# Kernel tuning notes

Measured on AMD Instinct MI355X. Metric: run time of the kernel, lower is better.

Reference implementation:

```python
import jax, jax.numpy as jnp
import numpy as np

N_CHEM = 200000
N_DIS = 200000
D = 256
L = 2  # num_layers
R = 4  # relations: 0=cause(chem->dis),1=relate(chem->dis),2=rev_relate(dis->chem),3=child(dis->dis)
E = 500000


def setup_inputs() -> dict:
    key = jax.random.key(0)
    ks = jax.random.split(key, 12)
    x_chem = jax.random.normal(ks[0], (N_CHEM, D), dtype=jnp.float32)
    x_dis = jax.random.normal(ks[1], (N_DIS, D), dtype=jnp.float32)
    ei_cause = jax.random.randint(ks[2], (2, E), 0, N_CHEM, dtype=jnp.int32)
    ei_relate = jax.random.randint(ks[3], (2, E), 0, N_CHEM, dtype=jnp.int32)
    ei_rev = jax.random.randint(ks[4], (2, E), 0, N_DIS, dtype=jnp.int32)
    ei_child = jax.random.randint(ks[5], (2, E), 0, N_DIS, dtype=jnp.int32)
    scale = 1.0 / np.sqrt(D)
    # PyG SAGEConv params per (layer, relation): lin_l (W+b, applied to mean-aggregated
    # neighbors) and lin_r (W only, applied to destination/root features).
    Wl = jax.random.normal(ks[6], (L, R, D, D), dtype=jnp.float32) * scale
    bl = jnp.zeros((L, R, D), dtype=jnp.float32)
    Wr = jax.random.normal(ks[7], (L, R, D, D), dtype=jnp.float32) * scale
    return {"x_chem": x_chem, "x_dis": x_dis, "Wl": Wl, "bl": bl, "Wr": Wr,
            "ei_cause": ei_cause, "ei_relate": ei_relate, "ei_rev": ei_rev,
            "ei_child": ei_child}


def _sage(x_src, x_dst, ei, Wl, bl, Wr, n_dst):
    # SAGEConv: lin_l(mean_{j in N(i)} x_j) + lin_r(x_i)
    src, dst = ei[0], ei[1]
    msg = jnp.take(x_src, src, axis=0)                      # [E, D] gather
    s = jax.ops.segment_sum(msg, dst, num_segments=n_dst)   # [n_dst, D]
    cnt = jax.ops.segment_sum(jnp.ones((ei.shape[1],), x_src.dtype), dst,
                              num_segments=n_dst)
    mean = s / jnp.maximum(cnt, 1.0)[:, None]               # zero-degree -> 0
    return mean @ Wl + bl + x_dst @ Wr


def _hetero_layer(x_chem, x_dis, Wl, bl, Wr, ei_cause, ei_relate, ei_rev, ei_child):
    # HeteroConv(aggr='sum'): sum conv outputs per destination node type.
    out_dis = (_sage(x_chem, x_dis, ei_cause, Wl[0], bl[0], Wr[0], N_DIS)
               + _sage(x_chem, x_dis, ei_relate, Wl[1], bl[1], Wr[1], N_DIS)
               + _sage(x_dis, x_dis, ei_child, Wl[3], bl[3], Wr[3], N_DIS))
    out_chem = _sage(x_dis, x_chem, ei_rev, Wl[2], bl[2], Wr[2], N_CHEM)
    return out_chem, out_dis


def reference(x_chem, x_dis, Wl, bl, Wr, ei_cause, ei_relate, ei_rev, ei_child):
    # layers[:-1]: conv -> relu -> dropout(p=0, identity)
    for l in range(L - 1):
        x_chem, x_dis = _hetero_layer(x_chem, x_dis, Wl[l], bl[l], Wr[l],
                                      ei_cause, ei_relate, ei_rev, ei_child)
        x_chem = jax.nn.relu(x_chem)
        x_dis = jax.nn.relu(x_dis)
    # last layer: conv only
    x_chem, x_dis = _hetero_layer(x_chem, x_dis, Wl[L - 1], bl[L - 1], Wr[L - 1],
                                  ei_cause, ei_relate, ei_rev, ei_child)
    return x_chem, x_dis
```

## Files before the change

### kernel.cpp

```cpp
#include <hip/hip_runtime.h>

#define D_FEAT 256
constexpr int N_CHEM = 200000;
constexpr int N_DIS  = 200000;
constexpr int N_EDGE = 500000;
constexpr int NROWS  = 200000;
constexpr int NPAD   = 200064;

typedef _Float16 f16x8 __attribute__((ext_vector_type(8)));
typedef _Float16 f16x4 __attribute__((ext_vector_type(4)));
typedef float    f32x4 __attribute__((ext_vector_type(4)));

__device__ __forceinline__ void gload_lds16(const void* g, void* l) {
    __builtin_amdgcn_global_load_lds(
        (const __attribute__((address_space(1))) void*)g,
        (__attribute__((address_space(3))) void*)l, 16, 0, 0);
}

__global__ __launch_bounds__(256) void counti_k(const int* __restrict__ ei,
                                                int* __restrict__ cnt, int nE) {
    int e = blockIdx.x * 256 + threadIdx.x;
    if (e < nE) atomicAdd(&cnt[ei[nE + e]], 1);
}

__global__ __launch_bounds__(256) void scan1_k(const int* __restrict__ cnt,
                                               int* __restrict__ offs,
                                               int* __restrict__ bsums, int n) {
    __shared__ int s[256];
    const int t = threadIdx.x;
    const int i = blockIdx.x * 256 + t;
    const int v = (i < n) ? cnt[i] : 0;
    s[t] = v;
    __syncthreads();
#pragma unroll
    for (int d = 1; d < 256; d <<= 1) {
        const int x = (t >= d) ? s[t - d] : 0;
        __syncthreads();
        s[t] += x;
        __syncthreads();
    }
    if (i < n) offs[i] = s[t] - v;
    if (t == 255) bsums[blockIdx.x] = s[255];
}

__global__ __launch_bounds__(1024) void scan2_k(int* __restrict__ bsums, int nb) {
    __shared__ int s[1024];
    const int t = threadIdx.x;
    const int v = (t < nb) ? bsums[t] : 0;
    s[t] = v;
    __syncthreads();
#pragma unroll
    for (int d = 1; d < 1024; d <<= 1) {
        const int x = (t >= d) ? s[t - d] : 0;
        __syncthreads();
        s[t] += x;
        __syncthreads();
    }
    if (t < nb) bsums[t] = s[t] - v;
}

__global__ __launch_bounds__(256) void scan3_k(int* __restrict__ offs,
                                               int* __restrict__ cursor,
                                               const int* __restrict__ bsums, int n) {
    const int i = blockIdx.x * 256 + threadIdx.x;
    if (i < n) {
        const int v = offs[i] + bsums[blockIdx.x];
        offs[i] = v;
        cursor[i] = v;
    }
}

__global__ __launch_bounds__(256) void fill_k(const int* __restrict__ ei,
                                              int* __restrict__ cursor,
                                              int* __restrict__ csr, int nE) {
    int e = blockIdx.x * 256 + threadIdx.x;
    if (e < nE) {
        const int d = ei[nE + e];
        const int p = atomicAdd(&cursor[d], 1);
        csr[p] = ei[e];
    }
}

__global__ __launch_bounds__(256) void wt_k(const float* __restrict__ Wl,
                                            const float* __restrict__ Wr,
                                            const float* __restrict__ bl,
                                            _Float16* __restrict__ WT_dis,
                                            _Float16* __restrict__ WT_chem,
                                            float* __restrict__ bsum, int l) {
    const int idx = blockIdx.x * 256 + threadIdx.x;
    const float* Wl_l = Wl + (size_t)l * 4 * 65536;
    const float* Wr_l = Wr + (size_t)l * 4 * 65536;
    if (idx < 262144) {
        const int n = idx >> 10, k = idx & 1023, seg = k >> 8, kk = k & 255;
        float v;
        if (seg == 0)
            v = Wr_l[kk * 256 + n] + Wr_l[65536 + kk * 256 + n] + Wr_l[3 * 65536 + kk * 256 + n];
        else if (seg == 1) v = Wl_l[kk * 256 + n];
        else if (seg == 2) v = Wl_l[65536 + kk * 256 + n];
        else               v = Wl_l[3 * 65536 + kk * 256 + n];
        WT_dis[(size_t)l * 262144 + idx] = (_Float16)v;
    } else if (idx < 393216) {
        const int li = idx - 262144;
        const int n = li >> 9, k = li & 511, seg = k >> 8, kk = k & 255;
        const float v = (seg == 0) ? Wr_l[2 * 65536 + kk * 256 + n]
                                   : Wl_l[2 * 65536 + kk * 256 + n];
        WT_chem[(size_t)l * 131072 + li] = (_Float16)v;
    } else if (idx < 393216 + 256) {
        const int n = idx - 393216;
        const float* b = bl + (size_t)l * 1024;
        bsum[l * 256 + n] = b[n] + b[256 + n] + b[3 * 256 + n];
    }
}

__global__ __launch_bounds__(256) void cvt16_k(const float* __restrict__ in,
                                               _Float16* __restrict__ out, int n4) {
    int i = blockIdx.x * 256 + threadIdx.x;
    if (i < n4) {
        const float4 v = reinterpret_cast<const float4*>(in)[i];
        f16x4 o;
        o[0] = (_Float16)v.x; o[1] = (_Float16)v.y;
        o[2] = (_Float16)v.z; o[3] = (_Float16)v.w;
        reinterpret_cast<f16x4*>(out)[i] = o;
    }
}

__global__ __launch_bounds__(256) void gather_k(const _Float16* __restrict__ x,
                                                const int* __restrict__ csr,
                                                const int* __restrict__ offs,
                                                const int* __restrict__ cnt,
                                                _Float16* __restrict__ agg,
                                                int base, int rows) {
    const int wid = threadIdx.x >> 6;
    const int lane = threadIdx.x & 63;
    const int grp = lane >> 4;
    const int li  = lane & 15;
    const int lrow = blockIdx.x * 16 + wid * 4 + grp;
    if (lrow >= rows) return;
    const int row = base + lrow;
    const int start = offs[row];
    const int n = cnt[row];
    float a0[8] = {0,0,0,0,0,0,0,0}, a1[8] = {0,0,0,0,0,0,0,0};
    const _Float16* xb = x + li * 16;
    for (int j = 0; j < n; ++j) {
        const int s = csr[start + j];
        const f16x8 v0 = *reinterpret_cast<const f16x8*>(xb + (size_t)s * D_FEAT);
        const f16x8 v1 = *reinterpret_cast<const f16x8*>(xb + (size_t)s * D_FEAT + 8);
#pragma unroll
        for (int q = 0; q < 8; ++q) { a0[q] += (float)v0[q]; a1[q] += (float)v1[q]; }
    }
    const float inv = 1.0f / fmaxf((float)n, 1.0f);
    f16x8 o0, o1;
#pragma unroll
    for (int q = 0; q < 8; ++q) {
        o0[q] = (_Float16)(a0[q] * inv);
        o1[q] = (_Float16)(a1[q] * inv);
    }
    _Float16* ap = agg + (size_t)lrow * D_FEAT + li * 16;
    *reinterpret_cast<f16x8*>(ap) = o0;
    *reinterpret_cast<f16x8*>(ap + 8) = o1;
}

template <int NSEG, bool RELU_OUT>
__global__ __launch_bounds__(256) void gemml_k(
    const _Float16* __restrict__ A0, const _Float16* __restrict__ A1,
    const _Float16* __restrict__ A2, const _Float16* __restrict__ A3,
    const _Float16* __restrict__ WT, const float* __restrict__ bias,
    float* __restrict__ Cf, _Float16* __restrict__ Ch, int vrows) {
    constexpr int KT = NSEG * 256;
    constexpr int NS = KT / 64;
    __shared__ _Float16 Asl[2][128 * 64];
    __shared__ _Float16 Bsl[2][128 * 64];
    const int t = threadIdx.x;
    const int w = t >> 6, l = t & 63;
    const int wm = w & 1, wn = w >> 1;
    const int fr = l & 15, ko = (l >> 4) << 3;
    const int row0 = blockIdx.x * 128;
    const int col0 = blockIdx.y * 128;

    f32x4 acc[4][4];
#pragma unroll
    for (int m = 0; m < 4; ++m)
#pragma unroll
        for (int n = 0; n < 4; ++n) acc[m][n] = f32x4{0.f, 0.f, 0.f, 0.f};

    const int srow = t >> 3;
    const int schk = t & 7;
    const int gchk = schk ^ (srow & 7);
    const int rsw  = (fr & 7) << 3;

    auto STAGE = [&](int buf, int ks) {
        const int seg = ks >> 2;
        const _Float16* Ab = (seg == 0) ? A0 : ((seg == 1) ? A1 : ((seg == 2) ? A2 : A3));
        const int kofs = ((ks & 3) << 6) + gchk * 8;
#pragma unroll
        for (int is = 0; is < 4; ++is) {
            gload_lds16(Ab + (size_t)(row0 + is * 32 + srow) * D_FEAT + kofs,
                        &Asl[buf][is * 2048 + w * 512]);
            gload_lds16(WT + (size_t)(col0 + is * 32 + srow) * KT + seg * 256 + kofs,
                        &Bsl[buf][is * 2048 + w * 512]);
        }
    };

    auto COMPUTE = [&](int buf) {
#pragma unroll
        for (int kk = 0; kk < 64; kk += 32) {
            f16x8 af[4], bf[4];
            const int ksw = (kk + ko) ^ rsw;
#pragma unroll
            for (int m = 0; m < 4; ++m)
                af[m] = *reinterpret_cast<const f16x8*>(&Asl[buf][(wm * 64 + m * 16 + fr) * 64 + ksw]);
#pragma unroll
            for (int n = 0; n < 4; ++n)
                bf[n] = *reinterpret_cast<const f16x8*>(&Bsl[buf][(wn * 64 + n * 16 + fr) * 64 + ksw]);
#pragma unroll
            for (int m = 0; m < 4; ++m)
#pragma unroll
                for (int n = 0; n < 4; ++n)
                    acc[m][n] = __builtin_amdgcn_mfma_f32_16x16x32_f16(af[m], bf[n], acc[m][n], 0, 0, 0);
        }
    };

    STAGE(0, 0);
    int cur = 0;
    for (int ks = 0; ks < NS - 1; ++ks) {
        STAGE(cur ^ 1, ks + 1);
        asm volatile("s_waitcnt vmcnt(8)" ::: "memory");
        __builtin_amdgcn_s_barrier();
        __builtin_amdgcn_sched_barrier(0);
        COMPUTE(cur);
        __builtin_amdgcn_sched_barrier(0);
        __builtin_amdgcn_s_barrier();
        __builtin_amdgcn_sched_barrier(0);
        cur ^= 1;
    }
    asm volatile("s_waitcnt vmcnt(0)" ::: "memory");
    __builtin_amdgcn_s_barrier();
    __builtin_amdgcn_sched_barrier(0);
    COMPUTE(cur);

    const int cro = (l >> 4) << 2;
#pragma unroll
    for (int n = 0; n < 4; ++n) {
        const int col = col0 + wn * 64 + n * 16 + fr;
        const float bi = bias[col];
#pragma unroll
        for (int m = 0; m < 4; ++m) {
            const int rbase = row0 + wm * 64 + m * 16 + cro;
#pragma unroll
            for (int j = 0; j < 4; ++j) {
                const int r = rbase + j;
                if (r < vrows) {
                    const float v = acc[m][n][j] + bi;
                    if constexpr (RELU_OUT)
                        Ch[(size_t)r * D_FEAT + col] = (_Float16)fmaxf(v, 0.f);
                    else
                        Cf[(size_t)r * D_FEAT + col] = v;
                }
            }
        }
    }
}

extern "C" void kernel_launch(void* const* d_in, const int* in_sizes, int n_in,
                              void* d_out, int out_size, void* d_ws, size_t ws_size,
                              hipStream_t stream) {
    const float* x_chem = (const float*)d_in[0];
    const float* x_dis  = (const float*)d_in[1];
    const float* Wl     = (const float*)d_in[2];
    const float* bl     = (const float*)d_in[3];
    const float* Wr     = (const float*)d_in[4];
    const int* ei[4] = {(const int*)d_in[5],
                        (const int*)d_in[6],
                        (const int*)d_in[7],
                        (const int*)d_in[8]};

    float* out_chem = (float*)d_out;
    float* out_dis  = out_chem + (size_t)N_CHEM * D_FEAT;

    constexpr size_t FB = (size_t)NPAD * D_FEAT * 2;
    char* w = (char*)d_ws;
    _Float16* h_chem  = (_Float16*)(w);
    _Float16* h_dis   = (_Float16*)(w + FB);
    _Float16* xb_chem = (_Float16*)(w + 2 * FB);
    _Float16* xb_dis  = (_Float16*)(w + 3 * FB);
    char* p = w + 4 * FB;
    int* csr    = (int*)(p);              p += 8000000;
    int* counts = (int*)(p);              p += 3200000;
    int* offs   = (int*)(p);              p += 3200000;
    int* cursor = (int*)(p);              p += 3200000;
    int* bsums  = (int*)(p);              p += 4096;
    _Float16* WT_dis  = (_Float16*)(p);   p += 1048576;
    _Float16* WT_chem = (_Float16*)(p);   p += 524288;
    float* bsum = (float*)(p);            p += 2048;
    _Float16* chunkbuf = (_Float16*)(p);

    const size_t FIXED = (size_t)(p - w);
    long long avail = (long long)ws_size - (long long)FIXED;
    int crp = 51200;
    if (avail < (long long)crp * 2048) {
        long long c = avail / 2048;
        if (c > NPAD) c = NPAD;
        crp = (int)(c & ~127LL);
        if (crp < 128) crp = 128;
    }

    const int cnt_grid = (N_EDGE + 255) / 256;
    const int scan_blocks = (NROWS + 255) / 256;

    hipMemsetAsync(counts, 0, 4 * NROWS * sizeof(int), stream);
    for (int r = 0; r < 4; ++r)
        counti_k<<<cnt_grid, 256, 0, stream>>>(ei[r], counts + r * NROWS, N_EDGE);
    for (int r = 0; r < 4; ++r) {
        scan1_k<<<scan_blocks, 256, 0, stream>>>(counts + r * NROWS, offs + r * NROWS, bsums, NROWS);
        scan2_k<<<1, 1024, 0, stream>>>(bsums, scan_blocks);
        scan3_k<<<scan_blocks, 256, 0, stream>>>(offs + r * NROWS, cursor + r * NROWS, bsums, NROWS);
        fill_k<<<cnt_grid, 256, 0, stream>>>(ei[r], cursor + r * NROWS, csr + r * N_EDGE, N_EDGE);
    }
    const int* csr_r[4];  const int* cnt_r[4];  const int* off_r[4];
    for (int r = 0; r < 4; ++r) {
        csr_r[r] = csr + r * N_EDGE;
        cnt_r[r] = counts + r * NROWS;
        off_r[r] = offs + r * NROWS;
    }

    wt_k<<<1538, 256, 0, stream>>>(Wl, Wr, bl, WT_dis, WT_chem, bsum, 0);
    wt_k<<<1538, 256, 0, stream>>>(Wl, Wr, bl, WT_dis, WT_chem, bsum, 1);
    const int cvt_grid = (NROWS * (D_FEAT / 4) + 255) / 256;
    cvt16_k<<<cvt_grid, 256, 0, stream>>>(x_chem, xb_chem, NROWS * (D_FEAT / 4));
    cvt16_k<<<cvt_grid, 256, 0, stream>>>(x_dis,  xb_dis,  NROWS * (D_FEAT / 4));

    _Float16* agg_c  = chunkbuf;
    _Float16* agg_r  = chunkbuf + (size_t)1 * crp * D_FEAT;
    _Float16* agg_ch = chunkbuf + (size_t)2 * crp * D_FEAT;
    _Float16* agg_rv = chunkbuf + (size_t)3 * crp * D_FEAT;

    for (int base = 0; base < NROWS; base += crp) {
        const int rows = (NROWS - base < crp) ? (NROWS - base) : crp;
        const int rows_pad = (rows + 127) & ~127;
        const int ggrid = (rows + 15) / 16;
        const dim3 mgrid(rows_pad / 128, 2);
        gather_k<<<ggrid, 256, 0, stream>>>(xb_chem, csr_r[0], off_r[0], cnt_r[0], agg_c, base, rows);
        gather_k<<<ggrid, 256, 0, stream>>>(xb_chem, csr_r[1], off_r[1], cnt_r[1], agg_r, base, rows);
        gather_k<<<ggrid, 256, 0, stream>>>(xb_dis,  csr_r[3], off_r[3], cnt_r[3], agg_ch, base, rows);
        gather_k<<<ggrid, 256, 0, stream>>>(xb_dis,  csr_r[2], off_r[2], cnt_r[2], agg_rv, base, rows);
        gemml_k<4, true><<<mgrid, 256, 0, stream>>>(
            xb_dis + (size_t)base * D_FEAT, agg_c, agg_r, agg_ch,
            WT_dis, bsum, nullptr, h_dis + (size_t)base * D_FEAT, rows);
        gemml_k<2, true><<<mgrid, 256, 0, stream>>>(
            xb_chem + (size_t)base * D_FEAT, agg_rv, nullptr, nullptr,
            WT_chem, bl + 2 * 256, nullptr, h_chem + (size_t)base * D_FEAT, rows);
    }

    for (int base = 0; base < NROWS; base += crp) {
        const int rows = (NROWS - base < crp) ? (NROWS - base) : crp;
        const int rows_pad = (rows + 127) & ~127;
        const int ggrid = (rows + 15) / 16;
        const dim3 mgrid(rows_pad / 128, 2);
        gather_k<<<ggrid, 256, 0, stream>>>(h_chem, csr_r[0], off_r[0], cnt_r[0], agg_c, base, rows);
        gather_k<<<ggrid, 256, 0, stream>>>(h_chem, csr_r[1], off_r[1], cnt_r[1], agg_r, base, rows);
        gather_k<<<ggrid, 256, 0, stream>>>(h_dis,  csr_r[3], off_r[3], cnt_r[3], agg_ch, base, rows);
        gather_k<<<ggrid, 256, 0, stream>>>(h_dis,  csr_r[2], off_r[2], cnt_r[2], agg_rv, base, rows);
        gemml_k<4, false><<<mgrid, 256, 0, stream>>>(
            h_dis + (size_t)base * D_FEAT, agg_c, agg_r, agg_ch,
            WT_dis + 262144, bsum + 256, out_dis + (size_t)base * D_FEAT, nullptr, rows);
        gemml_k<2, false><<<mgrid, 256, 0, stream>>>(
            h_chem + (size_t)base * D_FEAT, agg_rv, nullptr, nullptr,
            WT_chem + 131072, bl + 6 * 256, out_chem + (size_t)base * D_FEAT, nullptr, rows);
    }
}
```

Before: 1.921 ms.

## Batch CSR construction across relations and unroll gather loop by two

The per-relation count, scan and fill kernels are merged into single launches over all four relations, with one global scan over the concatenated counts. scan2 now handles four elements per thread so it can cover the larger block-sum array. Weight-transpose and fp16 conversion launches are merged through a 2D grid. The gather loop is unrolled by two so two neighbor rows are in flight at once. The aim is to cut kernel-launch and serialization overhead in preprocessing and to raise memory-level parallelism in the gather, at the cost of slightly more register pressure.

After: 1.825 ms. -5.0%, faster.

```diff
diff --git a/kernel.cpp b/kernel.cpp
--- a/kernel.cpp
+++ b/kernel.cpp
@@ -6,6 +6,8 @@
 constexpr int N_EDGE = 500000;
 constexpr int NROWS  = 200000;
 constexpr int NPAD   = 200064;
+constexpr int NCNT   = 4 * NROWS;
+constexpr int NEALL  = 4 * N_EDGE;
 
 typedef _Float16 f16x8 __attribute__((ext_vector_type(8)));
 typedef _Float16 f16x4 __attribute__((ext_vector_type(4)));
@@ -17,10 +19,16 @@
         (__attribute__((address_space(3))) void*)l, 16, 0, 0);
 }
 
-__global__ __launch_bounds__(256) void counti_k(const int* __restrict__ ei,
-                                                int* __restrict__ cnt, int nE) {
-    int e = blockIdx.x * 256 + threadIdx.x;
-    if (e < nE) atomicAdd(&cnt[ei[nE + e]], 1);
+__global__ __launch_bounds__(256) void counti_all_k(
+    const int* __restrict__ e0, const int* __restrict__ e1,
+    const int* __restrict__ e2, const int* __restrict__ e3,
+    int* __restrict__ cnt) {
+    const int g = blockIdx.x * 256 + threadIdx.x;
+    if (g >= NEALL) return;
+    const int r = g / N_EDGE;
+    const int le = g - r * N_EDGE;
+    const int* e = (r == 0) ? e0 : (r == 1) ? e1 : (r == 2) ? e2 : e3;
+    atomicAdd(&cnt[r * NROWS + e[N_EDGE + le]], 1);
 }
 
 __global__ __launch_bounds__(256) void scan1_k(const int* __restrict__ cnt,
@@ -46,8 +54,15 @@
 __global__ __launch_bounds__(1024) void scan2_k(int* __restrict__ bsums, int nb) {
     __shared__ int s[1024];
     const int t = threadIdx.x;
-    const int v = (t < nb) ? bsums[t] : 0;
-    s[t] = v;
+    int v[4];
+    int sum = 0;
+#pragma unroll
+    for (int q = 0; q < 4; ++q) {
+        const int i = t * 4 + q;
+        v[q] = (i < nb) ? bsums[i] : 0;
+        sum += v[q];
+    }
+    s[t] = sum;
     __syncthreads();
 #pragma unroll
     for (int d = 1; d < 1024; d <<= 1) {
@@ -56,7 +71,16 @@
         s[t] += x;
         __syncthreads();
     }
-    if (t < nb) bsums[t] = s[t] - v;
+    int base = s[t] - sum;
+#pragma unroll
+    for (int q = 0; q < 4; ++q) {
+        const int i = t * 4 + q;
+        if (i < nb) {
+            const int tmp = v[q];
+            bsums[i] = base;
+            base += tmp;
+        }
+    }
 }
 
 __global__ __launch_bounds__(256) void scan3_k(int* __restrict__ offs,
@@ -70,15 +94,18 @@
     }
 }
 
-__global__ __launch_bounds__(256) void fill_k(const int* __restrict__ ei,
-                                              int* __restrict__ cursor,
-                                              int* __restrict__ csr, int nE) {
-    int e = blockIdx.x * 256 + threadIdx.x;
-    if (e < nE) {
-        const int d = ei[nE + e];
-        const int p = atomicAdd(&cursor[d], 1);
-        csr[p] = ei[e];
-    }
+__global__ __launch_bounds__(256) void fill_all_k(
+    const int* __restrict__ e0, const int* __restrict__ e1,
+    const int* __restrict__ e2, const int* __restrict__ e3,
+    int* __restrict__ cursor, int* __restrict__ csr) {
+    const int g = blockIdx.x * 256 + threadIdx.x;
+    if (g >= NEALL) return;
+    const int r = g / N_EDGE;
+    const int le = g - r * N_EDGE;
+    const int* e = (r == 0) ? e0 : (r == 1) ? e1 : (r == 2) ? e2 : e3;
+    const int d = e[N_EDGE + le];
+    const int p = atomicAdd(&cursor[r * NROWS + d], 1);
+    csr[p] = e[le];
 }
 
 __global__ __launch_bounds__(256) void wt_k(const float* __restrict__ Wl,
@@ -86,8 +113,9 @@
                                             const float* __restrict__ bl,
                                             _Float16* __restrict__ WT_dis,
                                             _Float16* __restrict__ WT_chem,
-                                            float* __restrict__ bsum, int l) {
+                                            float* __restrict__ bsum) {
     const int idx = blockIdx.x * 256 + threadIdx.x;
+    const int l = blockIdx.y;
     const float* Wl_l = Wl + (size_t)l * 4 * 65536;
     const float* Wr_l = Wr + (size_t)l * 4 * 65536;
     if (idx < 262144) {
@@ -112,9 +140,13 @@
     }
 }
 
-__global__ __launch_bounds__(256) void cvt16_k(const float* __restrict__ in,
-                                               _Float16* __restrict__ out, int n4) {
-    int i = blockIdx.x * 256 + threadIdx.x;
+__global__ __launch_bounds__(256) void cvt2_k(const float* __restrict__ in0,
+                                              _Float16* __restrict__ out0,
+                                              const float* __restrict__ in1,
+                                              _Float16* __restrict__ out1, int n4) {
+    const int i = blockIdx.x * 256 + threadIdx.x;
+    const float* in = blockIdx.y ? in1 : in0;
+    _Float16* out = blockIdx.y ? out1 : out0;
     if (i < n4) {
         const float4 v = reinterpret_cast<const float4*>(in)[i];
         f16x4 o;
@@ -141,12 +173,26 @@
     const int n = cnt[row];
     float a0[8] = {0,0,0,0,0,0,0,0}, a1[8] = {0,0,0,0,0,0,0,0};
     const _Float16* xb = x + li * 16;
-    for (int j = 0; j < n; ++j) {
-        const int s = csr[start + j];
-        const f16x8 v0 = *reinterpret_cast<const f16x8*>(xb + (size_t)s * D_FEAT);
-        const f16x8 v1 = *reinterpret_cast<const f16x8*>(xb + (size_t)s * D_FEAT + 8);
-#pragma unroll
-        for (int q = 0; q < 8; ++q) { a0[q] += (float)v0[q]; a1[q] += (float)v1[q]; }
+    int j = 0;
+    for (; j + 2 <= n; j += 2) {
+        const int s0 = csr[start + j];
+        const int s1 = csr[start + j + 1];
+        const f16x8 u0 = *reinterpret_cast<const f16x8*>(xb + (size_t)s0 * D_FEAT);
+        const f16x8 u1 = *reinterpret_cast<const f16x8*>(xb + (size_t)s0 * D_FEAT + 8);
+        const f16x8 w0 = *reinterpret_cast<const f16x8*>(xb + (size_t)s1 * D_FEAT);
+        const f16x8 w1 = *reinterpret_cast<const f16x8*>(xb + (size_t)s1 * D_FEAT + 8);
+#pragma unroll
+        for (int q = 0; q < 8; ++q) {
+            a0[q] += (float)u0[q]; a1[q] += (float)u1[q];
+            a0[q] += (float)w0[q]; a1[q] += (float)w1[q];
+        }
+    }
+    if (j < n) {
+        const int s0 = csr[start + j];
+        const f16x8 u0 = *reinterpret_cast<const f16x8*>(xb + (size_t)s0 * D_FEAT);
+        const f16x8 u1 = *reinterpret_cast<const f16x8*>(xb + (size_t)s0 * D_FEAT + 8);
+#pragma unroll
+        for (int q = 0; q < 8; ++q) { a0[q] += (float)u0[q]; a1[q] += (float)u1[q]; }
     }
     const float inv = 1.0f / fmaxf((float)n, 1.0f);
     f16x8 o0, o1;
@@ -288,7 +334,7 @@
     int* counts = (int*)(p);              p += 3200000;
     int* offs   = (int*)(p);              p += 3200000;
     int* cursor = (int*)(p);              p += 3200000;
-    int* bsums  = (int*)(p);              p += 4096;
+    int* bsums  = (int*)(p);              p += 16384;
     _Float16* WT_dis  = (_Float16*)(p);   p += 1048576;
     _Float16* WT_chem = (_Float16*)(p);   p += 524288;
     float* bsum = (float*)(p);            p += 2048;
@@ -304,30 +350,25 @@
         if (crp < 128) crp = 128;
     }
 
-    const int cnt_grid = (N_EDGE + 255) / 256;
-    const int scan_blocks = (NROWS + 255) / 256;
-
-    hipMemsetAsync(counts, 0, 4 * NROWS * sizeof(int), stream);
-    for (int r = 0; r < 4; ++r)
-        counti_k<<<cnt_grid, 256, 0, stream>>>(ei[r], counts + r * NROWS, N_EDGE);
+    const int eall_grid = (NEALL + 255) / 256;
+    const int scan_blocks = (NCNT + 255) / 256;
+    hipMemsetAsync(counts, 0, NCNT * sizeof(int), stream);
+    counti_all_k<<<eall_grid, 256, 0, stream>>>(ei[0], ei[1], ei[2], ei[3], counts);
+    scan1_k<<<scan_blocks, 256, 0, stream>>>(counts, offs, bsums, NCNT);
+    scan2_k<<<1, 1024, 0, stream>>>(bsums, scan_blocks);
+    scan3_k<<<scan_blocks, 256, 0, stream>>>(offs, cursor, bsums, NCNT);
+    fill_all_k<<<eall_grid, 256, 0, stream>>>(ei[0], ei[1], ei[2], ei[3], cursor, csr);
+
+    const int* cnt_r[4];  const int* off_r[4];
     for (int r = 0; r < 4; ++r) {
-        scan1_k<<<scan_blocks, 256, 0, stream>>>(counts + r * NROWS, offs + r * NROWS, bsums, NROWS);
-        scan2_k<<<1, 1024, 0, stream>>>(bsums, scan_blocks);
-        scan3_k<<<scan_blocks, 256, 0, stream>>>(offs + r * NROWS, cursor + r * NROWS, bsums, NROWS);
-        fill_k<<<cnt_grid, 256, 0, stream>>>(ei[r], cursor + r * NROWS, csr + r * N_EDGE, N_EDGE);
-    }
-    const int* csr_r[4];  const int* cnt_r[4];  const int* off_r[4];
-    for (int r = 0; r < 4; ++r) {
-        csr_r[r] = csr + r * N_EDGE;
         cnt_r[r] = counts + r * NROWS;
         off_r[r] = offs + r * NROWS;
     }
 
-    wt_k<<<1538, 256, 0, stream>>>(Wl, Wr, bl, WT_dis, WT_chem, bsum, 0);
-    wt_k<<<1538, 256, 0, stream>>>(Wl, Wr, bl, WT_dis, WT_chem, bsum, 1);
+    wt_k<<<dim3(1538, 2), 256, 0, stream>>>(Wl, Wr, bl, WT_dis, WT_chem, bsum);
     const int cvt_grid = (NROWS * (D_FEAT / 4) + 255) / 256;
-    cvt16_k<<<cvt_grid, 256, 0, stream>>>(x_chem, xb_chem, NROWS * (D_FEAT / 4));
-    cvt16_k<<<cvt_grid, 256, 0, stream>>>(x_dis,  xb_dis,  NROWS * (D_FEAT / 4));
+    cvt2_k<<<dim3(cvt_grid, 2), 256, 0, stream>>>(x_chem, xb_chem, x_dis, xb_dis,
+                                                  NROWS * (D_FEAT / 4));
 
     _Float16* agg_c  = chunkbuf;
     _Float16* agg_r  = chunkbuf + (size_t)1 * crp * D_FEAT;
@@ -339,10 +380,10 @@
         const int rows_pad = (rows + 127) & ~127;
         const int ggrid = (rows + 15) / 16;
         const dim3 mgrid(rows_pad / 128, 2);
-        gather_k<<<ggrid, 256, 0, stream>>>(xb_chem, csr_r[0], off_r[0], cnt_r[0], agg_c, base, rows);
-        gather_k<<<ggrid, 256, 0, stream>>>(xb_chem, csr_r[1], off_r[1], cnt_r[1], agg_r, base, rows);
-        gather_k<<<ggrid, 256, 0, stream>>>(xb_dis,  csr_r[3], off_r[3], cnt_r[3], agg_ch, base, rows);
-        gather_k<<<ggrid, 256, 0, stream>>>(xb_dis,  csr_r[2], off_r[2], cnt_r[2], agg_rv, base, rows);
+        gather_k<<<ggrid, 256, 0, stream>>>(xb_chem, csr, off_r[0], cnt_r[0], agg_c, base, rows);
+        gather_k<<<ggrid, 256, 0, stream>>>(xb_chem, csr, off_r[1], cnt_r[1], agg_r, base, rows);
+        gather_k<<<ggrid, 256, 0, stream>>>(xb_dis,  csr, off_r[3], cnt_r[3], agg_ch, base, rows);
+        gather_k<<<ggrid, 256, 0, stream>>>(xb_dis,  csr, off_r[2], cnt_r[2], agg_rv, base, rows);
         gemml_k<4, true><<<mgrid, 256, 0, stream>>>(
             xb_dis + (size_t)base * D_FEAT, agg_c, agg_r, agg_ch,
             WT_dis, bsum, nullptr, h_dis + (size_t)base * D_FEAT, rows);
@@ -356,10 +397,10 @@
         const int rows_pad = (rows + 127) & ~127;
         const int ggrid = (rows + 15) / 16;
         const dim3 mgrid(rows_pad / 128, 2);
-        gather_k<<<ggrid, 256, 0, stream>>>(h_chem, csr_r[0], off_r[0], cnt_r[0], agg_c, base, rows);
-        gather_k<<<ggrid, 256, 0, stream>>>(h_chem, csr_r[1], off_r[1], cnt_r[1], agg_r, base, rows);
-        gather_k<<<ggrid, 256, 0, stream>>>(h_dis,  csr_r[3], off_r[3], cnt_r[3], agg_ch, base, rows);
-        gather_k<<<ggrid, 256, 0, stream>>>(h_dis,  csr_r[2], off_r[2], cnt_r[2], agg_rv, base, rows);
+        gather_k<<<ggrid, 256, 0, stream>>>(h_chem, csr, off_r[0], cnt_r[0], agg_c, base, rows);
+        gather_k<<<ggrid, 256, 0, stream>>>(h_chem, csr, off_r[1], cnt_r[1], agg_r, base, rows);
+        gather_k<<<ggrid, 256, 0, stream>>>(h_dis,  csr, off_r[3], cnt_r[3], agg_ch, base, rows);
+        gather_k<<<ggrid, 256, 0, stream>>>(h_dis,  csr, off_r[2], cnt_r[2], agg_rv, base, rows);
         gemml_k<4, false><<<mgrid, 256, 0, stream>>>(
             h_dis + (size_t)base * D_FEAT, agg_c, agg_r, agg_ch,
             WT_dis + 262144, bsum + 256, out_dis + (size_t)base * D_FEAT, nullptr, rows);
```
